# Optimization experiments

Hardware: AMD Instinct MI355X
Metric: run time of the kernel (lower is better)

Reference implementation:

```python
import jax, jax.numpy as jnp
import numpy as np
from jax.scipy.special import logsumexp

B, N, D, NUM_CLASSES = 8192, 8192, 256, 64
TEMPERATURE = 1.0


def setup_inputs() -> dict:
    key = jax.random.key(0)
    k1, k2, k3, k4 = jax.random.split(key, 4)
    return {
        "text_features": jax.random.normal(k1, (B, D), dtype=jnp.float32),
        "image_features": jax.random.normal(k2, (N, D), dtype=jnp.float32),
        "t_label": jax.random.randint(k3, (B,), 0, NUM_CLASSES),
        "i_targets": jax.random.randint(k4, (N,), 0, NUM_CLASSES),
    }


def reference(text_features, image_features, t_label, i_targets):
    # logits[i,j] = <text_i, image_j> / T   -> [B, N]
    logits = jnp.matmul(text_features, image_features.T) / TEMPERATURE
    mask = t_label[:, None] == i_targets[None, :]  # [B, N] positives
    neg_inf = jnp.array(-jnp.inf, dtype=logits.dtype)
    # per-row logsumexp over positives of -logits, and over negatives of +logits
    lse_p = logsumexp(jnp.where(mask, -logits, neg_inf), axis=1)
    lse_n = logsumexp(jnp.where(mask, neg_inf, logits), axis=1)
    loss = jnp.mean(jax.nn.softplus(lse_n + lse_p))
    return loss
```

## Files before the change

kernel.cpp:

```cpp
#include <hip/hip_runtime.h>
#include <hip/hip_bf16.h>


#define B_ROWS   8192
#define N_COLS   8192
#define DIM      256
#define CSPLIT   32
#define NTILES   ((N_COLS / CSPLIT) / 32)
#define BLK_ROWS 128
#define THREADS  256

typedef __attribute__((ext_vector_type(8))) short bf16x8;
typedef __attribute__((ext_vector_type(4))) float f32x4;

#if __has_builtin(__builtin_amdgcn_exp2f)
#define EXP2F(x) __builtin_amdgcn_exp2f(x)
#else
#define EXP2F(x) exp2f(x)
#endif
#if __has_builtin(__builtin_amdgcn_logf)
#define LOG2F(x) __builtin_amdgcn_logf(x)
#else
#define LOG2F(x) log2f(x)
#endif

__device__ __forceinline__ unsigned short f2bf(float f) {
    union { float f; unsigned u; } c; c.f = f;
    return (unsigned short)((c.u + 0x7FFFu + ((c.u >> 16) & 1u)) >> 16);
}

__global__ void cvt_all_kernel(const float* __restrict__ text,
                               const float* __restrict__ img,
                               unsigned short* __restrict__ Abf,
                               unsigned short* __restrict__ Bt,
                               float* __restrict__ gsum) {
    const int i = blockIdx.x * blockDim.x + threadIdx.x;
    if (i < 4096) {
        reinterpret_cast<float4*>(gsum)[i] = float4{0.f, 0.f, 0.f, 0.f};
    }
    if (i < 262144) {
        const float4* src = reinterpret_cast<const float4*>(text) + i * 2;
        float4 v0 = src[0], v1 = src[1];
        unsigned short s[8];
        s[0] = f2bf(v0.x); s[1] = f2bf(v0.y); s[2] = f2bf(v0.z); s[3] = f2bf(v0.w);
        s[4] = f2bf(v1.x); s[5] = f2bf(v1.y); s[6] = f2bf(v1.z); s[7] = f2bf(v1.w);
        reinterpret_cast<bf16x8*>(Abf)[i] = *reinterpret_cast<const bf16x8*>(s);
    } else {
        const int C = i - 262144;
        const int g = C >> 10, c = C & 1023;
        const int col = g * 32 + (c & 31);
        const int k8  = c >> 5;
        const float4* src =
            reinterpret_cast<const float4*>(img + (size_t)col * DIM + k8 * 8);
        float4 v0 = src[0], v1 = src[1];
        unsigned short s[8];
        s[0] = f2bf(v0.x); s[1] = f2bf(v0.y); s[2] = f2bf(v0.z); s[3] = f2bf(v0.w);
        s[4] = f2bf(v1.x); s[5] = f2bf(v1.y); s[6] = f2bf(v1.z); s[7] = f2bf(v1.w);
        reinterpret_cast<bf16x8*>(Bt)[C] = *reinterpret_cast<const bf16x8*>(s);
    }
}

__launch_bounds__(THREADS, 3)
__global__ void fused_gemm_lse(const unsigned short* __restrict__ Abf,
                               const unsigned short* __restrict__ Bt,
                               const int* __restrict__ tlab,
                               const int* __restrict__ itgt,
                               float* __restrict__ gsum_p,
                               float* __restrict__ gsum_n) {
    __shared__ char lds[2 * 16384] __attribute__((aligned(128)));

    const int tid  = threadIdx.x;
    const int lane = tid & 63;
    const int wave = tid >> 6;
    const int l15  = lane & 15;
    const int q    = lane >> 4;
    const int rb   = blockIdx.x * BLK_ROWS + wave * 32;
    const int cb0  = blockIdx.y * (N_COLS / CSPLIT);

    bf16x8 afrag0[8], afrag1[8];
    const bf16x8* arow0 =
        reinterpret_cast<const bf16x8*>(Abf + (size_t)(rb + l15) * DIM) + q;
    const bf16x8* arow1 =
        reinterpret_cast<const bf16x8*>(Abf + (size_t)(rb + 16 + l15) * DIM) + q;
#pragma unroll
    for (int ks = 0; ks < 8; ++ks) {
        afrag0[ks] = arow0[ks * 4];
        afrag1[ks] = arow1[ks * 4];
    }

    int rowcls0[4], rowcls1[4];
#pragma unroll
    for (int j = 0; j < 4; ++j) {
        rowcls0[j] = tlab[rb + q * 4 + j];
        rowcls1[j] = tlab[rb + 16 + q * 4 + j];
    }

    float sump0[4] = {0, 0, 0, 0}, sumn0[4] = {0, 0, 0, 0};
    float sump1[4] = {0, 0, 0, 0}, sumn1[4] = {0, 0, 0, 0};

    const char* bsrc = (const char*)Bt
        + ((size_t)blockIdx.y * NTILES) * 16384 + tid * 16;
    char* ldsd = lds + tid * 16;

#define STAGE(T, BUF) do {                                                    \
    _Pragma("unroll")                                                         \
    for (int i_ = 0; i_ < 4; ++i_)                                            \
        __builtin_amdgcn_global_load_lds(                                     \
            (const __attribute__((address_space(1))) unsigned int*)           \
                (bsrc + (size_t)(T) * 16384 + i_ * 4096),                     \
            (__attribute__((address_space(3))) unsigned int*)                 \
                (ldsd + (BUF) * 16384 + i_ * 4096),                           \
            16, 0, 0);                                                        \
} while (0)

    const float L2E = 1.4426950408889634f;
    const float C2  = 72.0f;

    STAGE(0, 0);

    for (int t = 0; t < NTILES; ++t) {
        __syncthreads();

        if (t + 1 < NTILES) STAGE(t + 1, (t + 1) & 1);

        const int cc0 = itgt[cb0 + t * 32 + l15];
        const int cc1 = itgt[cb0 + t * 32 + 16 + l15];

        f32x4 acc00 = {0, 0, 0, 0}, acc01 = {0, 0, 0, 0};
        f32x4 acc10 = {0, 0, 0, 0}, acc11 = {0, 0, 0, 0};
        const char* bb = lds + (t & 1) * 16384 + q * 512 + l15 * 16;
#pragma unroll
        for (int ks = 0; ks < 8; ++ks) {
            bf16x8 b0 = *reinterpret_cast<const bf16x8*>(bb + ks * 2048);
            bf16x8 b1 = *reinterpret_cast<const bf16x8*>(bb + ks * 2048 + 256);
            acc00 = __builtin_amdgcn_mfma_f32_16x16x32_bf16(afrag0[ks], b0,
                                                            acc00, 0, 0, 0);
            acc01 = __builtin_amdgcn_mfma_f32_16x16x32_bf16(afrag0[ks], b1,
                                                            acc01, 0, 0, 0);
            acc10 = __builtin_amdgcn_mfma_f32_16x16x32_bf16(afrag1[ks], b0,
                                                            acc10, 0, 0, 0);
            acc11 = __builtin_amdgcn_mfma_f32_16x16x32_bf16(afrag1[ks], b1,
                                                            acc11, 0, 0, 0);
        }

#pragma unroll
        for (int j = 0; j < 4; ++j) {
            {
                const float x = acc00[j];
                const bool  p = (rowcls0[j] == cc0);
                const float e = EXP2F(__builtin_fmaf(x, p ? -L2E : L2E, -C2));
                sump0[j] += p ? e : 0.f;
                sumn0[j] += p ? 0.f : e;
            }
            {
                const float x = acc01[j];
                const bool  p = (rowcls0[j] == cc1);
                const float e = EXP2F(__builtin_fmaf(x, p ? -L2E : L2E, -C2));
                sump0[j] += p ? e : 0.f;
                sumn0[j] += p ? 0.f : e;
            }
            {
                const float x = acc10[j];
                const bool  p = (rowcls1[j] == cc0);
                const float e = EXP2F(__builtin_fmaf(x, p ? -L2E : L2E, -C2));
                sump1[j] += p ? e : 0.f;
                sumn1[j] += p ? 0.f : e;
            }
            {
                const float x = acc11[j];
                const bool  p = (rowcls1[j] == cc1);
                const float e = EXP2F(__builtin_fmaf(x, p ? -L2E : L2E, -C2));
                sump1[j] += p ? e : 0.f;
                sumn1[j] += p ? 0.f : e;
            }
        }
    }
#undef STAGE

#pragma unroll
    for (int j = 0; j < 4; ++j) {
        float vp0 = sump0[j], vn0 = sumn0[j];
        float vp1 = sump1[j], vn1 = sumn1[j];
#pragma unroll
        for (int m = 1; m < 16; m <<= 1) {
            vp0 += __shfl_xor(vp0, m, 64);
            vn0 += __shfl_xor(vn0, m, 64);
            vp1 += __shfl_xor(vp1, m, 64);
            vn1 += __shfl_xor(vn1, m, 64);
        }
        if (l15 == 0) {
            const int row0 = rb + q * 4 + j;
            atomicAdd(&gsum_p[row0], vp0);
            atomicAdd(&gsum_n[row0], vn0);
            const int row1 = rb + 16 + q * 4 + j;
            atomicAdd(&gsum_p[row1], vp1);
            atomicAdd(&gsum_n[row1], vn1);
        }
    }
}

__global__ void finalize_kernel(const float* __restrict__ gsum_p,
                                const float* __restrict__ gsum_n,
                                float* __restrict__ out) {
    __shared__ float red[1024];
    const float LN2 = 0.6931471805599453f;
    const float C2  = 72.0f;
    float acc = 0.f;
    for (int i = threadIdx.x; i < B_ROWS; i += 1024) {
        float zp = (LOG2F(gsum_p[i]) + C2) * LN2;
        float zn = (LOG2F(gsum_n[i]) + C2) * LN2;
        float z  = zp + zn;
        float sp = fmaxf(z, 0.f) + log1pf(expf(-fabsf(z)));
        acc += sp;
    }
    red[threadIdx.x] = acc;
    __syncthreads();
    for (int s = 512; s > 0; s >>= 1) {
        if ((int)threadIdx.x < s) red[threadIdx.x] += red[threadIdx.x + s];
        __syncthreads();
    }
    if (threadIdx.x == 0) out[0] = red[0] / (float)B_ROWS;
}

extern "C" void kernel_launch(void* const* d_in, const int* in_sizes, int n_in,
                              void* d_out, int out_size, void* d_ws, size_t ws_size,
                              hipStream_t stream) {
    const float* text = (const float*)d_in[0];
    const float* img  = (const float*)d_in[1];
    const int* tlab   = (const int*)d_in[2];
    const int* itgt   = (const int*)d_in[3];
    float* out        = (float*)d_out;

    char* ws = (char*)d_ws;
    unsigned short* Abf = (unsigned short*)(ws);
    unsigned short* Bt  = (unsigned short*)(ws + (size_t)B_ROWS * DIM * 2);
    float* gsum_p = (float*)(ws + (size_t)(B_ROWS + N_COLS) * DIM * 2);
    float* gsum_n = gsum_p + B_ROWS;

    cvt_all_kernel<<<(2 * 262144) / 256, 256, 0, stream>>>(text, img, Abf, Bt,
                                                           gsum_p);

    dim3 grid(B_ROWS / BLK_ROWS, CSPLIT);
    fused_gemm_lse<<<grid, THREADS, 0, stream>>>(Abf, Bt, tlab, itgt,
                                                 gsum_p, gsum_n);

    finalize_kernel<<<1, 1024, 0, stream>>>(gsum_p, gsum_n, out);
}
```

Baseline: 68.31 us.

## Load B fragments straight to registers with split-K double buffering, drop LDS

Replaces the shared-memory staging of B tiles (global_load_lds plus __syncthreads) with per-wave direct global loads into two register buffers, each holding half of the K range. Loads for the next tile are issued between the MFMA halves to overlap memory with compute. The tile loop is fully unrolled and the occupancy hint drops from 3 to 2 blocks to leave room for the extra registers. The negative-sum update is simplified to accumulate every exponential, and the positive sum is subtracted once at the end. This removes block barriers and LDS traffic, but each wave now fetches the same B data separately, and the subtraction can lose precision.

```diff
diff --git a/kernel.cpp b/kernel.cpp
--- a/kernel.cpp
+++ b/kernel.cpp
@@ -60,15 +60,13 @@
     }
 }
 
-__launch_bounds__(THREADS, 3)
+__launch_bounds__(THREADS, 2)
 __global__ void fused_gemm_lse(const unsigned short* __restrict__ Abf,
                                const unsigned short* __restrict__ Bt,
                                const int* __restrict__ tlab,
                                const int* __restrict__ itgt,
                                float* __restrict__ gsum_p,
                                float* __restrict__ gsum_n) {
-    __shared__ char lds[2 * 16384] __attribute__((aligned(128)));
-
     const int tid  = threadIdx.x;
     const int lane = tid & 63;
     const int wave = tid >> 6;
@@ -98,50 +96,53 @@
     float sump0[4] = {0, 0, 0, 0}, sumn0[4] = {0, 0, 0, 0};
     float sump1[4] = {0, 0, 0, 0}, sumn1[4] = {0, 0, 0, 0};
 
-    const char* bsrc = (const char*)Bt
-        + ((size_t)blockIdx.y * NTILES) * 16384 + tid * 16;
-    char* ldsd = lds + tid * 16;
-
-#define STAGE(T, BUF) do {                                                    \
+    const char* bp = (const char*)Bt
+        + ((size_t)blockIdx.y * NTILES) * 16384 + q * 512 + l15 * 16;
+
+    bf16x8 bA[8], bB[8];
+
+#define LOADH(buf, T, H) do {                                                 \
     _Pragma("unroll")                                                         \
-    for (int i_ = 0; i_ < 4; ++i_)                                            \
-        __builtin_amdgcn_global_load_lds(                                     \
-            (const __attribute__((address_space(1))) unsigned int*)           \
-                (bsrc + (size_t)(T) * 16384 + i_ * 4096),                     \
-            (__attribute__((address_space(3))) unsigned int*)                 \
-                (ldsd + (BUF) * 16384 + i_ * 4096),                           \
-            16, 0, 0);                                                        \
+    for (int k_ = 0; k_ < 4; ++k_) {                                          \
+        buf[2 * k_] = *reinterpret_cast<const bf16x8*>(                       \
+            bp + (size_t)(T) * 16384 + ((H) * 4 + k_) * 2048);                \
+        buf[2 * k_ + 1] = *reinterpret_cast<const bf16x8*>(                   \
+            bp + (size_t)(T) * 16384 + ((H) * 4 + k_) * 2048 + 256);          \
+    }                                                                         \
+} while (0)
+
+#define MFMAH(buf, H) do {                                                    \
+    _Pragma("unroll")                                                         \
+    for (int k_ = 0; k_ < 4; ++k_) {                                          \
+        acc00 = __builtin_amdgcn_mfma_f32_16x16x32_bf16(                      \
+            afrag0[(H) * 4 + k_], buf[2 * k_], acc00, 0, 0, 0);               \
+        acc01 = __builtin_amdgcn_mfma_f32_16x16x32_bf16(                      \
+            afrag0[(H) * 4 + k_], buf[2 * k_ + 1], acc01, 0, 0, 0);           \
+        acc10 = __builtin_amdgcn_mfma_f32_16x16x32_bf16(                      \
+            afrag1[(H) * 4 + k_], buf[2 * k_], acc10, 0, 0, 0);               \
+        acc11 = __builtin_amdgcn_mfma_f32_16x16x32_bf16(                      \
+            afrag1[(H) * 4 + k_], buf[2 * k_ + 1], acc11, 0, 0, 0);           \
+    }                                                                         \
 } while (0)
 
     const float L2E = 1.4426950408889634f;
     const float C2  = 72.0f;
 
-    STAGE(0, 0);
-
+    LOADH(bA, 0, 0);
+    LOADH(bB, 0, 1);
+
+#pragma unroll
     for (int t = 0; t < NTILES; ++t) {
-        __syncthreads();
-
-        if (t + 1 < NTILES) STAGE(t + 1, (t + 1) & 1);
-
         const int cc0 = itgt[cb0 + t * 32 + l15];
         const int cc1 = itgt[cb0 + t * 32 + 16 + l15];
 
         f32x4 acc00 = {0, 0, 0, 0}, acc01 = {0, 0, 0, 0};
         f32x4 acc10 = {0, 0, 0, 0}, acc11 = {0, 0, 0, 0};
-        const char* bb = lds + (t & 1) * 16384 + q * 512 + l15 * 16;
-#pragma unroll
-        for (int ks = 0; ks < 8; ++ks) {
-            bf16x8 b0 = *reinterpret_cast<const bf16x8*>(bb + ks * 2048);
-            bf16x8 b1 = *reinterpret_cast<const bf16x8*>(bb + ks * 2048 + 256);
-            acc00 = __builtin_amdgcn_mfma_f32_16x16x32_bf16(afrag0[ks], b0,
-                                                            acc00, 0, 0, 0);
-            acc01 = __builtin_amdgcn_mfma_f32_16x16x32_bf16(afrag0[ks], b1,
-                                                            acc01, 0, 0, 0);
-            acc10 = __builtin_amdgcn_mfma_f32_16x16x32_bf16(afrag1[ks], b0,
-                                                            acc10, 0, 0, 0);
-            acc11 = __builtin_amdgcn_mfma_f32_16x16x32_bf16(afrag1[ks], b1,
-                                                            acc11, 0, 0, 0);
-        }
+
+        MFMAH(bA, 0);
+        if (t + 1 < NTILES) LOADH(bA, t + 1, 0);
+        MFMAH(bB, 1);
+        if (t + 1 < NTILES) LOADH(bB, t + 1, 1);
 
 #pragma unroll
         for (int j = 0; j < 4; ++j) {
@@ -149,33 +150,34 @@
                 const float x = acc00[j];
                 const bool  p = (rowcls0[j] == cc0);
                 const float e = EXP2F(__builtin_fmaf(x, p ? -L2E : L2E, -C2));
+                sumn0[j] += e;
                 sump0[j] += p ? e : 0.f;
-                sumn0[j] += p ? 0.f : e;
             }
             {
                 const float x = acc01[j];
                 const bool  p = (rowcls0[j] == cc1);
                 const float e = EXP2F(__builtin_fmaf(x, p ? -L2E : L2E, -C2));
+                sumn0[j] += e;
                 sump0[j] += p ? e : 0.f;
-                sumn0[j] += p ? 0.f : e;
             }
             {
                 const float x = acc10[j];
                 const bool  p = (rowcls1[j] == cc0);
                 const float e = EXP2F(__builtin_fmaf(x, p ? -L2E : L2E, -C2));
+                sumn1[j] += e;
                 sump1[j] += p ? e : 0.f;
-                sumn1[j] += p ? 0.f : e;
             }
             {
                 const float x = acc11[j];
                 const bool  p = (rowcls1[j] == cc1);
                 const float e = EXP2F(__builtin_fmaf(x, p ? -L2E : L2E, -C2));
+                sumn1[j] += e;
                 sump1[j] += p ? e : 0.f;
-                sumn1[j] += p ? 0.f : e;
             }
         }
     }
-#undef STAGE
+#undef LOADH
+#undef MFMAH
 
 #pragma unroll
     for (int j = 0; j < 4; ++j) {
@@ -191,10 +193,10 @@
         if (l15 == 0) {
             const int row0 = rb + q * 4 + j;
             atomicAdd(&gsum_p[row0], vp0);
-            atomicAdd(&gsum_n[row0], vn0);
+            atomicAdd(&gsum_n[row0], vn0 - vp0);
             const int row1 = rb + 16 + q * 4 + j;
             atomicAdd(&gsum_p[row1], vp1);
-            atomicAdd(&gsum_n[row1], vn1);
+            atomicAdd(&gsum_n[row1], vn1 - vp1);
         }
     }
 }
```

New measurement: 146.4 us. +114.4%, slower.
